# Kernel optimization log

Measured on AMD Instinct MI355X. Metric: run time of the kernel, lower is better.

The kernel has to match this reference:

```python
import jax, jax.numpy as jnp
import numpy as np

N_NODES = 100000
N_EDGES = 800000
DIMS = [(768, 64), (64, 32), (32, 16), (16, 5)]


def setup_inputs() -> dict:
    key = jax.random.key(0)
    ks = jax.random.split(key, 3 + 3 * len(DIMS))
    inp = {
        "x": jax.random.normal(ks[0], (N_NODES, DIMS[0][0]), jnp.float32),
        "edge_index": jax.random.randint(ks[1], (2, N_EDGES), 0, N_NODES),
        "edge_weight": jax.random.uniform(ks[2], (N_EDGES,), jnp.float32),
    }
    for i, (di, do) in enumerate(DIMS, start=1):
        s = 1.0 / np.sqrt(di)
        k0, k1, k2 = ks[3 * i], ks[3 * i + 1], ks[3 * i + 2]
        inp[f"W{i}l"] = jax.random.uniform(k0, (di, do), jnp.float32, -s, s)
        inp[f"W{i}r"] = jax.random.uniform(k1, (di, do), jnp.float32, -s, s)
        inp[f"b{i}"] = jax.random.uniform(k2, (do,), jnp.float32, -s, s)
    return inp


def _sage_conv(h, src, dst, inv_deg, Wl, Wr, b):
    # SAGEConv (mean aggregation): lin_l(mean_{j->i} h_j) + lin_r(h_i)
    agg = jax.ops.segment_sum(h[src], dst, num_segments=h.shape[0]) * inv_deg[:, None]
    return agg @ Wl + h @ Wr + b


def reference(x, edge_index, edge_weight,
              W1l, W1r, b1, W2l, W2r, b2, W3l, W3r, b3, W4l, W4r, b4):
    # edge_weight is accepted (matches original forward) but PyG SAGEConv mean
    # aggregation ignores it. Dropout is identity (deterministic eval reference).
    src, dst = edge_index[0], edge_index[1]
    deg = jax.ops.segment_sum(jnp.ones((src.shape[0],), x.dtype), dst,
                              num_segments=x.shape[0])
    inv_deg = jnp.where(deg > 0, 1.0 / deg, 0.0)
    h = jax.nn.relu(_sage_conv(x, src, dst, inv_deg, W1l, W1r, b1))
    h = jax.nn.relu(_sage_conv(h, src, dst, inv_deg, W2l, W2r, b2))
    h = jax.nn.relu(_sage_conv(h, src, dst, inv_deg, W3l, W3r, b3))
    return _sage_conv(h, src, dst, inv_deg, W4l, W4r, b4)
```

## Files before the change

kernel.cpp:

```cpp
#include <hip/hip_runtime.h>

using half8 = __attribute__((ext_vector_type(8))) _Float16;
using f32x4 = __attribute__((ext_vector_type(4))) float;

typedef __attribute__((address_space(3))) unsigned int lds_uint;
typedef __attribute__((address_space(1))) const unsigned int glb_uint;
__device__ __forceinline__ void async_copy16(const void* g, void* l) {
  __builtin_amdgcn_global_load_lds((glb_uint*)g, (lds_uint*)l, 16, 0, 0);
}

__device__ __forceinline__ void raw_barrier() {
  asm volatile("" ::: "memory");
  __builtin_amdgcn_s_barrier();
  asm volatile("" ::: "memory");
}

__global__ void prep_zero_kernel(const float* __restrict__ W1l, const float* __restrict__ W1r,
                                 const float* __restrict__ W2l, const float* __restrict__ W2r,
                                 const float* __restrict__ W3l, const float* __restrict__ W3r,
                                 const float* __restrict__ W4l, const float* __restrict__ W4r,
                                 _Float16* __restrict__ w1, _Float16* __restrict__ w2,
                                 _Float16* __restrict__ w3, _Float16* __restrict__ w4,
                                 int4* __restrict__ zp, int n4) {
  int i = blockIdx.x * 256 + threadIdx.x;
  if (i < 98304) {
    int c = i / 768, k = i - c * 768;
    float v = (c < 64) ? W1l[k * 64 + c] : W1r[k * 64 + (c - 64)];
    w1[i] = (_Float16)v;
  } else if (i < 98304 + 4096) {
    int j = i - 98304;
    int c = j >> 6, k = j & 63;
    float v = (c < 32) ? W2l[k * 32 + c] : W2r[k * 32 + (c - 32)];
    w2[j] = (_Float16)v;
  } else if (i < 98304 + 4096 + 1024) {
    int j = i - (98304 + 4096);
    int c = j >> 5, k = j & 31;
    float v = (c < 16) ? W3l[k * 16 + c] : W3r[k * 16 + (c - 16)];
    w3[j] = (_Float16)v;
  } else if (i < 98304 + 4096 + 1024 + 512) {
    int j = i - (98304 + 4096 + 1024);
    int c = j >> 5, k = j & 31;
    float v = 0.f;
    if (k < 16) {
      if (c < 5) v = W4l[k * 5 + c];
      else if (c < 10) v = W4r[k * 5 + (c - 5)];
    }
    w4[j] = (_Float16)v;
  } else {
    int j = i - (98304 + 4096 + 1024 + 512);
    if (j < n4) zp[j] = make_int4(0, 0, 0, 0);
  }
}

__global__ void deg_kernel(const int* __restrict__ dst, int* __restrict__ cnt, int e) {
  int i = blockIdx.x * 256 + threadIdx.x;
  if (i < e) atomicAdd(&cnt[dst[i]], 1);
}

__global__ void scan1_kernel(const int* __restrict__ cnt, int* __restrict__ off,
                             int* __restrict__ bsum, float* __restrict__ invd, int nodes) {
  __shared__ int sh[256];
  int tid = threadIdx.x;
  int base = blockIdx.x * 1024 + tid * 4;
  int a0 = (base + 0 < nodes) ? cnt[base + 0] : 0;
  int a1 = (base + 1 < nodes) ? cnt[base + 1] : 0;
  int a2 = (base + 2 < nodes) ? cnt[base + 2] : 0;
  int a3 = (base + 3 < nodes) ? cnt[base + 3] : 0;
  if (base + 0 < nodes) invd[base + 0] = a0 > 0 ? 1.0f / (float)a0 : 0.f;
  if (base + 1 < nodes) invd[base + 1] = a1 > 0 ? 1.0f / (float)a1 : 0.f;
  if (base + 2 < nodes) invd[base + 2] = a2 > 0 ? 1.0f / (float)a2 : 0.f;
  if (base + 3 < nodes) invd[base + 3] = a3 > 0 ? 1.0f / (float)a3 : 0.f;
  int s3 = a0 + a1 + a2 + a3;
  sh[tid] = s3;
  __syncthreads();
  for (int d = 1; d < 256; d <<= 1) {
    int v = (tid >= d) ? sh[tid - d] : 0;
    __syncthreads();
    sh[tid] += v;
    __syncthreads();
  }
  int excl = sh[tid] - s3;
  if (base + 0 <= nodes) off[base + 0] = excl;
  if (base + 1 <= nodes) off[base + 1] = excl + a0;
  if (base + 2 <= nodes) off[base + 2] = excl + a0 + a1;
  if (base + 3 <= nodes) off[base + 3] = excl + a0 + a1 + a2;
  if (tid == 255) bsum[blockIdx.x] = sh[255];
}

__global__ void scan2_kernel(int* __restrict__ bsum, int nb) {
  __shared__ int sh[128];
  int tid = threadIdx.x;
  int v = (tid < nb) ? bsum[tid] : 0;
  sh[tid] = v;
  __syncthreads();
  for (int d = 1; d < 128; d <<= 1) {
    int u = (tid >= d) ? sh[tid - d] : 0;
    __syncthreads();
    sh[tid] += u;
    __syncthreads();
  }
  if (tid < nb) bsum[tid] = sh[tid] - v;
}

__global__ void scan3_kernel(int* __restrict__ off, const int* __restrict__ bsum, int ntot) {
  int i = blockIdx.x * 256 + threadIdx.x;
  if (i < ntot) off[i] += bsum[i >> 10];
}

__global__ __launch_bounds__(256, 3) void gemm1_sortfill_kernel(
    const float* __restrict__ x, const _Float16* __restrict__ w16,
    const float* __restrict__ bias, _Float16* __restrict__ p, _Float16* __restrict__ q,
    int n, int gemm_gb, const int* __restrict__ esrc, const int* __restrict__ edst,
    const int* __restrict__ off, int* __restrict__ cur, int* __restrict__ csr, int E) {
  if ((int)blockIdx.x >= gemm_gb) {
    int i = ((int)blockIdx.x - gemm_gb) * 256 + threadIdx.x;
    if (i < E) {
      int d = edst[i];
      int pos = atomicAdd(&cur[d], 1);
      csr[off[d] + pos] = esrc[i];
    }
    return;
  }
  constexpr int DI = 768, BK = 32, NT = DI / BK;
  __shared__ float aS[2][128 * BK];
  __shared__ _Float16 bS[2][128 * BK];
  int t = threadIdx.x;
  int lane = t & 63, w = t >> 6;
  int lm = lane & 15, lk = lane >> 4;
  int m0 = blockIdx.x * 128;

  const float* agp[4];
  int abase[4];
#pragma unroll
  for (int j = 0; j < 4; ++j) {
    int g = (j * 4 + w) * 64 + lane;
    int row = g >> 3, gi = g & 7;
    int gj = gi ^ (row & 7);
    int grow = m0 + row;
    if (grow >= n) grow = n - 1;
    agp[j] = x + (size_t)grow * DI + gj * 4;
    abase[j] = (j * 4 + w) * 256;
  }
  const _Float16* bgp[2];
  int bbase[2];
#pragma unroll
  for (int j = 0; j < 2; ++j) {
    int g = (j * 4 + w) * 64 + lane;
    int c = g >> 2, gi = g & 3;
    int gj = gi ^ ((c >> 1) & 3);
    bgp[j] = w16 + (size_t)c * DI + gj * 8;
    bbase[j] = (j * 4 + w) * 512;
  }

  f32x4 acc[2][8];
#pragma unroll
  for (int mi = 0; mi < 2; ++mi)
#pragma unroll
    for (int ni = 0; ni < 8; ++ni) acc[mi][ni] = (f32x4){0.f, 0.f, 0.f, 0.f};

  int r0l = w * 32 + lm, r1l = r0l + 16;
  int sw = lm & 7;
  int bsw = (lk ^ ((lm >> 1) & 3)) << 3;

  auto compute_tile = [&](const float* ab, const _Float16* bb) {
    f32x4 v0a = *(const f32x4*)(ab + r0l * 32 + (((lk * 2 + 0) ^ sw) << 2));
    f32x4 v0b = *(const f32x4*)(ab + r0l * 32 + (((lk * 2 + 1) ^ sw) << 2));
    f32x4 v1a = *(const f32x4*)(ab + r1l * 32 + (((lk * 2 + 0) ^ sw) << 2));
    f32x4 v1b = *(const f32x4*)(ab + r1l * 32 + (((lk * 2 + 1) ^ sw) << 2));
    half8 a0, a1;
#pragma unroll
    for (int j = 0; j < 4; ++j) {
      a0[j] = (_Float16)v0a[j]; a0[4 + j] = (_Float16)v0b[j];
      a1[j] = (_Float16)v1a[j]; a1[4 + j] = (_Float16)v1b[j];
    }
#pragma unroll
    for (int ni = 0; ni < 8; ++ni) {
      half8 b = *(const half8*)(bb + ni * 512 + lm * 32 + bsw);
      acc[0][ni] = __builtin_amdgcn_mfma_f32_16x16x32_f16(a0, b, acc[0][ni], 0, 0, 0);
      acc[1][ni] = __builtin_amdgcn_mfma_f32_16x16x32_f16(a1, b, acc[1][ni], 0, 0, 0);
    }
  };

#pragma unroll
  for (int j = 0; j < 4; ++j) async_copy16(agp[j], &aS[0][abase[j]]);
#pragma unroll
  for (int j = 0; j < 2; ++j) async_copy16(bgp[j], &bS[0][bbase[j]]);

  for (int ts = 0; ts < NT - 1; ++ts) {
    int cur2 = ts & 1;
    int kc = (ts + 1) * BK;
#pragma unroll
    for (int j = 0; j < 4; ++j) async_copy16(agp[j] + kc, &aS[cur2 ^ 1][abase[j]]);
#pragma unroll
    for (int j = 0; j < 2; ++j) async_copy16(bgp[j] + kc, &bS[cur2 ^ 1][bbase[j]]);
    asm volatile("s_waitcnt vmcnt(6)" ::: "memory");
    raw_barrier();
    compute_tile(aS[cur2], bS[cur2]);
    raw_barrier();
  }
  asm volatile("s_waitcnt vmcnt(0)" ::: "memory");
  raw_barrier();
  compute_tile(aS[(NT - 1) & 1], bS[(NT - 1) & 1]);

#pragma unroll
  for (int mi = 0; mi < 2; ++mi)
#pragma unroll
    for (int ni = 0; ni < 8; ++ni) {
      int col = ni * 16 + lm;
#pragma unroll
      for (int j = 0; j < 4; ++j) {
        int row = m0 + w * 32 + mi * 16 + lk * 4 + j;
        if (row < n) {
          float v = acc[mi][ni][j];
          if (col < 64) p[(size_t)row * 64 + col] = (_Float16)v;
          else q[(size_t)row * 64 + (col - 64)] = (_Float16)(v + bias[col - 64]);
        }
      }
    }
}

template <int DIR, int DIP, int PSI, int NC, int NCR, int DO, int PSO>
__global__ __launch_bounds__(512) void fused_agg_gemm_kernel(
    const _Float16* __restrict__ pin, const _Float16* __restrict__ qin,
    const int* __restrict__ off, const int* __restrict__ csr, const float* __restrict__ invd,
    const _Float16* __restrict__ w16, const float* __restrict__ bias,
    _Float16* __restrict__ pout, _Float16* __restrict__ qout, int n) {
  constexpr int SP = DIP + 8;
  constexpr int C8 = DIR / 8;
  constexpr int ACT = (C8 >= 4) ? 4 : C8;
  constexpr int CQ = C8 / ACT;
  constexpr int NF = NC / 16;
  __shared__ _Float16 hs[128 * SP];
  int t = threadIdx.x;
  int node_l = t >> 2, q4 = t & 3;
  int node = blockIdx.x * 128 + node_l;

  if (node < n) {
    if (q4 < ACT) {
      int e0 = off[node], e1 = off[node + 1];
      const half8* p8 = (const half8*)pin;
      float s[CQ][8];
#pragma unroll
      for (int c = 0; c < CQ; ++c)
#pragma unroll
        for (int j = 0; j < 8; ++j) s[c][j] = 0.f;
      int e = e0;
      for (; e + 4 <= e1; e += 4) {
        int i0 = csr[e], i1 = csr[e + 1], i2 = csr[e + 2], i3 = csr[e + 3];
        half8 v0[CQ], v1[CQ], v2[CQ], v3[CQ];
#pragma unroll
        for (int c = 0; c < CQ; ++c) v0[c] = p8[(size_t)i0 * PSI + q4 * CQ + c];
#pragma unroll
        for (int c = 0; c < CQ; ++c) v1[c] = p8[(size_t)i1 * PSI + q4 * CQ + c];
#pragma unroll
        for (int c = 0; c < CQ; ++c) v2[c] = p8[(size_t)i2 * PSI + q4 * CQ + c];
#pragma unroll
        for (int c = 0; c < CQ; ++c) v3[c] = p8[(size_t)i3 * PSI + q4 * CQ + c];
#pragma unroll
        for (int c = 0; c < CQ; ++c)
#pragma unroll
          for (int j = 0; j < 8; ++j) {
            s[c][j] += (float)v0[c][j];
            s[c][j] += (float)v1[c][j];
            s[c][j] += (float)v2[c][j];
            s[c][j] += (float)v3[c][j];
          }
      }
      for (; e < e1; ++e) {
        int i0 = csr[e];
#pragma unroll
        for (int c = 0; c < CQ; ++c) {
          half8 v = p8[(size_t)i0 * PSI + q4 * CQ + c];
#pragma unroll
          for (int j = 0; j < 8; ++j) s[c][j] += (float)v[j];
        }
      }
      float id = invd[node];
#pragma unroll
      for (int c = 0; c < CQ; ++c) {
        half8 qv = ((const half8*)qin)[(size_t)node * PSI + q4 * CQ + c];
        half8 o;
#pragma unroll
        for (int j = 0; j < 8; ++j) o[j] = (_Float16)fmaxf(s[c][j] * id + (float)qv[j], 0.f);
        *(half8*)(hs + node_l * SP + (q4 * CQ + c) * 8) = o;
      }
    } else if (DIP > DIR && (q4 - ACT) < (DIP - DIR) / 8) {
      half8 z = {};
      *(half8*)(hs + node_l * SP + (C8 + (q4 - ACT)) * 8) = z;
    }
  }
  asm volatile("s_waitcnt lgkmcnt(0)" ::: "memory");
  __builtin_amdgcn_sched_barrier(0);

  int lane = t & 63, w = t >> 6;
  int lm = lane & 15, lk = lane >> 4;
  int row_l = w * 16 + lm;
  const _Float16* wp = w16 + (size_t)lm * DIP + lk * 8;
  f32x4 acc[NF];
#pragma unroll
  for (int ni = 0; ni < NF; ++ni) acc[ni] = (f32x4){0.f, 0.f, 0.f, 0.f};
#pragma unroll
  for (int kc = 0; kc < DIP; kc += 32) {
    half8 a = *(const half8*)(hs + row_l * SP + kc + lk * 8);
#pragma unroll
    for (int ni = 0; ni < NF; ++ni) {
      half8 b = *(const half8*)(wp + (size_t)ni * 16 * DIP + kc);
      acc[ni] = __builtin_amdgcn_mfma_f32_16x16x32_f16(a, b, acc[ni], 0, 0, 0);
    }
  }
#pragma unroll
  for (int ni = 0; ni < NF; ++ni) {
    int col = ni * 16 + lm;
    if (col >= NCR) continue;
#pragma unroll
    for (int j = 0; j < 4; ++j) {
      int row = blockIdx.x * 128 + w * 16 + lk * 4 + j;
      if (row < n) {
        float v = acc[ni][j];
        if (col < DO) pout[(size_t)row * PSO + col] = (_Float16)v;
        else qout[(size_t)row * PSO + (col - DO)] = (_Float16)(v + bias[col - DO]);
      }
    }
  }
}

__global__ __launch_bounds__(256) void aggregate_last_kernel(
    const _Float16* __restrict__ p, const _Float16* __restrict__ q,
    const int* __restrict__ off, const int* __restrict__ csr,
    const float* __restrict__ invd, float* __restrict__ out, int n) {
  int node = blockIdx.x * 256 + threadIdx.x;
  if (node >= n) return;
  int e0 = off[node], e1 = off[node + 1];
  const half8* p8 = (const half8*)p;
  float s[8];
#pragma unroll
  for (int j = 0; j < 8; ++j) s[j] = 0.f;
  int e = e0;
  for (; e + 4 <= e1; e += 4) {
    half8 v0 = p8[csr[e]];
    half8 v1 = p8[csr[e + 1]];
    half8 v2 = p8[csr[e + 2]];
    half8 v3 = p8[csr[e + 3]];
#pragma unroll
    for (int j = 0; j < 8; ++j) {
      s[j] += (float)v0[j];
      s[j] += (float)v1[j];
      s[j] += (float)v2[j];
      s[j] += (float)v3[j];
    }
  }
  for (; e < e1; ++e) {
    half8 v = p8[csr[e]];
#pragma unroll
    for (int j = 0; j < 8; ++j) s[j] += (float)v[j];
  }
  float id = invd[node];
  half8 qv = ((const half8*)q)[node];
#pragma unroll
  for (int j = 0; j < 5; ++j) out[(size_t)node * 5 + j] = s[j] * id + (float)qv[j];
}

extern "C" void kernel_launch(void* const* d_in, const int* in_sizes, int n_in,
                              void* d_out, int out_size, void* d_ws, size_t ws_size,
                              hipStream_t stream) {
  const float* x = (const float*)d_in[0];
  const int* ei = (const int*)d_in[1];
  const int E = in_sizes[1] / 2;
  const int* esrc = ei;
  const int* edst = ei + E;
  const float* W1l = (const float*)d_in[3];
  const float* W1r = (const float*)d_in[4];
  const float* b1 = (const float*)d_in[5];
  const float* W2l = (const float*)d_in[6];
  const float* W2r = (const float*)d_in[7];
  const float* b2 = (const float*)d_in[8];
  const float* W3l = (const float*)d_in[9];
  const float* W3r = (const float*)d_in[10];
  const float* b3 = (const float*)d_in[11];
  const float* W4l = (const float*)d_in[12];
  const float* W4r = (const float*)d_in[13];
  const float* b4 = (const float*)d_in[14];
  const int N = in_sizes[0] / 768;
  float* out = (float*)d_out;
  (void)n_in; (void)out_size; (void)ws_size;

  char* base = (char*)d_ws;
  size_t o = 0;
  auto alloc = [&](size_t bytes) -> void* {
    void* ptr = base + o;
    o = (o + bytes + 255) & ~(size_t)255;
    return ptr;
  };
  int* cnt = (int*)alloc((size_t)2 * N * 4);
  int* cur = cnt + N;
  int* off = (int*)alloc((size_t)(N + 1) * 4);
  int* bsum = (int*)alloc(1024);
  int* csr = (int*)alloc((size_t)E * 4);
  float* invd = (float*)alloc((size_t)N * 4);
  _Float16* w1 = (_Float16*)alloc((size_t)128 * 768 * 2);
  _Float16* w2 = (_Float16*)alloc((size_t)64 * 64 * 2);
  _Float16* w3 = (_Float16*)alloc((size_t)32 * 32 * 2);
  _Float16* w4 = (_Float16*)alloc((size_t)16 * 32 * 2);
  _Float16* P1 = (_Float16*)alloc((size_t)N * 64 * 2);
  _Float16* Q1 = (_Float16*)alloc((size_t)N * 64 * 2);
  _Float16* P2 = (_Float16*)alloc((size_t)N * 32 * 2);
  _Float16* Q2 = (_Float16*)alloc((size_t)N * 32 * 2);
  _Float16* P3 = (_Float16*)alloc((size_t)N * 16 * 2);
  _Float16* Q3 = (_Float16*)alloc((size_t)N * 16 * 2);
  _Float16* P4 = (_Float16*)alloc((size_t)N * 8 * 2);
  _Float16* Q4 = (_Float16*)alloc((size_t)N * 8 * 2);

  const int n4 = (2 * N + 3) / 4;
  const int prep_tot = 98304 + 4096 + 1024 + 512 + n4;
  prep_zero_kernel<<<(prep_tot + 255) / 256, 256, 0, stream>>>(
      W1l, W1r, W2l, W2r, W3l, W3r, W4l, W4r, w1, w2, w3, w4, (int4*)cnt, n4);

  deg_kernel<<<(E + 255) / 256, 256, 0, stream>>>(edst, cnt, E);
  const int nb = (N + 1 + 1023) / 1024;
  scan1_kernel<<<nb, 256, 0, stream>>>(cnt, off, bsum, invd, N);
  scan2_kernel<<<1, 128, 0, stream>>>(bsum, nb);
  scan3_kernel<<<(N + 1 + 255) / 256, 256, 0, stream>>>(off, bsum, N + 1);

  const int gemm_gb = (N + 127) / 128;
  const int sf_gb = (E + 255) / 256;
  gemm1_sortfill_kernel<<<gemm_gb + sf_gb, 256, 0, stream>>>(
      x, w1, b1, P1, Q1, N, gemm_gb, esrc, edst, off, cur, csr, E);

  const int gb = (N + 127) / 128;
  fused_agg_gemm_kernel<64, 64, 8, 64, 64, 32, 32>
      <<<gb, 512, 0, stream>>>(P1, Q1, off, csr, invd, w2, b2, P2, Q2, N);
  fused_agg_gemm_kernel<32, 32, 4, 32, 32, 16, 16>
      <<<gb, 512, 0, stream>>>(P2, Q2, off, csr, invd, w3, b3, P3, Q3, N);
  fused_agg_gemm_kernel<16, 32, 2, 16, 10, 5, 8>
      <<<gb, 512, 0, stream>>>(P3, Q3, off, csr, invd, w4, b4, P4, Q4, N);
  aggregate_last_kernel<<<(N + 255) / 256, 256, 0, stream>>>(P4, Q4, off, csr, invd, out, N);
}
```

Before: 239.9 us.

## Make gemm1 warps independent with per-wave LDS staging and no barriers

Restructures the first-layer GEMM so each wave owns a private 16-row slice and its own double-buffered LDS copies of both the A and B tiles. This removes all block-level barriers in the K loop. Each wave now waits only on its own vmcnt counter before computing. The block tile shrinks from 128 to 64 rows and launch bounds drop to 2 blocks per SM. The cost is that every wave redundantly loads the full 128x32 weight tile, which quadruples B traffic into LDS, raises LDS usage per block, and lowers occupancy.

New measurement: 300.8 us. +25.4%, slower.

```diff
diff --git a/kernel.cpp b/kernel.cpp
--- a/kernel.cpp
+++ b/kernel.cpp
@@ -7,12 +7,6 @@
 typedef __attribute__((address_space(1))) const unsigned int glb_uint;
 __device__ __forceinline__ void async_copy16(const void* g, void* l) {
   __builtin_amdgcn_global_load_lds((glb_uint*)g, (lds_uint*)l, 16, 0, 0);
-}
-
-__device__ __forceinline__ void raw_barrier() {
-  asm volatile("" ::: "memory");
-  __builtin_amdgcn_s_barrier();
-  asm volatile("" ::: "memory");
 }
 
 __global__ void prep_zero_kernel(const float* __restrict__ W1l, const float* __restrict__ W1r,
@@ -107,7 +101,7 @@
   if (i < ntot) off[i] += bsum[i >> 10];
 }
 
-__global__ __launch_bounds__(256, 3) void gemm1_sortfill_kernel(
+__global__ __launch_bounds__(256, 2) void gemm1_sortfill_kernel(
     const float* __restrict__ x, const _Float16* __restrict__ w16,
     const float* __restrict__ bias, _Float16* __restrict__ p, _Float16* __restrict__ q,
     int n, int gemm_gb, const int* __restrict__ esrc, const int* __restrict__ edst,
@@ -122,101 +116,89 @@
     return;
   }
   constexpr int DI = 768, BK = 32, NT = DI / BK;
-  __shared__ float aS[2][128 * BK];
-  __shared__ _Float16 bS[2][128 * BK];
+  __shared__ float aS[4][2][512];
+  __shared__ _Float16 bS[4][2][4096];
   int t = threadIdx.x;
   int lane = t & 63, w = t >> 6;
   int lm = lane & 15, lk = lane >> 4;
-  int m0 = blockIdx.x * 128;
-
-  const float* agp[4];
-  int abase[4];
-#pragma unroll
-  for (int j = 0; j < 4; ++j) {
-    int g = (j * 4 + w) * 64 + lane;
+  int m0w = blockIdx.x * 64 + w * 16;
+
+  const float* agp[2];
+#pragma unroll
+  for (int j = 0; j < 2; ++j) {
+    int g = j * 64 + lane;
     int row = g >> 3, gi = g & 7;
     int gj = gi ^ (row & 7);
-    int grow = m0 + row;
+    int grow = m0w + row;
     if (grow >= n) grow = n - 1;
     agp[j] = x + (size_t)grow * DI + gj * 4;
-    abase[j] = (j * 4 + w) * 256;
-  }
-  const _Float16* bgp[2];
-  int bbase[2];
-#pragma unroll
-  for (int j = 0; j < 2; ++j) {
-    int g = (j * 4 + w) * 64 + lane;
+  }
+  const _Float16* bgp[8];
+#pragma unroll
+  for (int j = 0; j < 8; ++j) {
+    int g = j * 64 + lane;
     int c = g >> 2, gi = g & 3;
     int gj = gi ^ ((c >> 1) & 3);
     bgp[j] = w16 + (size_t)c * DI + gj * 8;
-    bbase[j] = (j * 4 + w) * 512;
-  }
-
-  f32x4 acc[2][8];
-#pragma unroll
-  for (int mi = 0; mi < 2; ++mi)
-#pragma unroll
-    for (int ni = 0; ni < 8; ++ni) acc[mi][ni] = (f32x4){0.f, 0.f, 0.f, 0.f};
-
-  int r0l = w * 32 + lm, r1l = r0l + 16;
+  }
+
+  f32x4 acc[8];
+#pragma unroll
+  for (int ni = 0; ni < 8; ++ni) acc[ni] = (f32x4){0.f, 0.f, 0.f, 0.f};
+
   int sw = lm & 7;
   int bsw = (lk ^ ((lm >> 1) & 3)) << 3;
 
-  auto compute_tile = [&](const float* ab, const _Float16* bb) {
-    f32x4 v0a = *(const f32x4*)(ab + r0l * 32 + (((lk * 2 + 0) ^ sw) << 2));
-    f32x4 v0b = *(const f32x4*)(ab + r0l * 32 + (((lk * 2 + 1) ^ sw) << 2));
-    f32x4 v1a = *(const f32x4*)(ab + r1l * 32 + (((lk * 2 + 0) ^ sw) << 2));
-    f32x4 v1b = *(const f32x4*)(ab + r1l * 32 + (((lk * 2 + 1) ^ sw) << 2));
-    half8 a0, a1;
+  auto stage = [&](int buf, int kc) {
+#pragma unroll
+    for (int j = 0; j < 2; ++j) async_copy16(agp[j] + kc, &aS[w][buf][j * 256]);
+#pragma unroll
+    for (int j = 0; j < 8; ++j) async_copy16(bgp[j] + kc, &bS[w][buf][j * 512]);
+  };
+
+  auto compute_tile = [&](int buf) {
+    const float* ab = aS[w][buf];
+    const _Float16* bb = bS[w][buf];
+    f32x4 v0a = *(const f32x4*)(ab + lm * 32 + (((lk * 2 + 0) ^ sw) << 2));
+    f32x4 v0b = *(const f32x4*)(ab + lm * 32 + (((lk * 2 + 1) ^ sw) << 2));
+    half8 a0;
 #pragma unroll
     for (int j = 0; j < 4; ++j) {
-      a0[j] = (_Float16)v0a[j]; a0[4 + j] = (_Float16)v0b[j];
-      a1[j] = (_Float16)v1a[j]; a1[4 + j] = (_Float16)v1b[j];
+      a0[j] = (_Float16)v0a[j];
+      a0[4 + j] = (_Float16)v0b[j];
     }
 #pragma unroll
     for (int ni = 0; ni < 8; ++ni) {
       half8 b = *(const half8*)(bb + ni * 512 + lm * 32 + bsw);
-      acc[0][ni] = __builtin_amdgcn_mfma_f32_16x16x32_f16(a0, b, acc[0][ni], 0, 0, 0);
-      acc[1][ni] = __builtin_amdgcn_mfma_f32_16x16x32_f16(a1, b, acc[1][ni], 0, 0, 0);
+      acc[ni] = __builtin_amdgcn_mfma_f32_16x16x32_f16(a0, b, acc[ni], 0, 0, 0);
     }
   };
 
-#pragma unroll
-  for (int j = 0; j < 4; ++j) async_copy16(agp[j], &aS[0][abase[j]]);
-#pragma unroll
-  for (int j = 0; j < 2; ++j) async_copy16(bgp[j], &bS[0][bbase[j]]);
-
-  for (int ts = 0; ts < NT - 1; ++ts) {
-    int cur2 = ts & 1;
-    int kc = (ts + 1) * BK;
-#pragma unroll
-    for (int j = 0; j < 4; ++j) async_copy16(agp[j] + kc, &aS[cur2 ^ 1][abase[j]]);
-#pragma unroll
-    for (int j = 0; j < 2; ++j) async_copy16(bgp[j] + kc, &bS[cur2 ^ 1][bbase[j]]);
-    asm volatile("s_waitcnt vmcnt(6)" ::: "memory");
-    raw_barrier();
-    compute_tile(aS[cur2], bS[cur2]);
-    raw_barrier();
-  }
-  asm volatile("s_waitcnt vmcnt(0)" ::: "memory");
-  raw_barrier();
-  compute_tile(aS[(NT - 1) & 1], bS[(NT - 1) & 1]);
-
-#pragma unroll
-  for (int mi = 0; mi < 2; ++mi)
-#pragma unroll
-    for (int ni = 0; ni < 8; ++ni) {
-      int col = ni * 16 + lm;
-#pragma unroll
-      for (int j = 0; j < 4; ++j) {
-        int row = m0 + w * 32 + mi * 16 + lk * 4 + j;
-        if (row < n) {
-          float v = acc[mi][ni][j];
-          if (col < 64) p[(size_t)row * 64 + col] = (_Float16)v;
-          else q[(size_t)row * 64 + (col - 64)] = (_Float16)(v + bias[col - 64]);
-        }
+  stage(0, 0);
+  for (int ts = 0; ts < NT; ++ts) {
+    if (ts + 1 < NT) {
+      stage((ts + 1) & 1, (ts + 1) * BK);
+      asm volatile("s_waitcnt vmcnt(10)" ::: "memory");
+    } else {
+      asm volatile("s_waitcnt vmcnt(0)" ::: "memory");
+    }
+    __builtin_amdgcn_sched_barrier(0);
+    compute_tile(ts & 1);
+  }
+
+#pragma unroll
+  for (int ni = 0; ni < 8; ++ni) {
+    int col = ni * 16 + lm;
+#pragma unroll
+    for (int j = 0; j < 4; ++j) {
+      int row = m0w + lk * 4 + j;
+      if (row < n) {
+        float v = acc[ni][j];
+        if (col < 64) p[(size_t)row * 64 + col] = (_Float16)v;
+        else q[(size_t)row * 64 + (col - 64)] = (_Float16)(v + bias[col - 64]);
       }
     }
+  }
 }
 
 template <int DIR, int DIP, int PSI, int NC, int NCR, int DO, int PSO>
@@ -421,7 +403,7 @@
   scan2_kernel<<<1, 128, 0, stream>>>(bsum, nb);
   scan3_kernel<<<(N + 1 + 255) / 256, 256, 0, stream>>>(off, bsum, N + 1);
 
-  const int gemm_gb = (N + 127) / 128;
+  const int gemm_gb = (N + 63) / 64;
   const int sf_gb = (E + 255) / 256;
   gemm1_sortfill_kernel<<<gemm_gb + sf_gb, 256, 0, stream>>>(
       x, w1, b1, P1, Q1, N, gemm_gb, esrc, edst, off, cur, csr, E);
```
